# Performance work log

Hardware: AMD Instinct MI355X
Metric: run time of the kernel (lower is better)

Reference implementation:

```python
import jax, jax.numpy as jnp
import numpy as np

N = 100000      # nodes
E = 1600000     # edges
HID = 128       # hidden_dim
HEADS = 4
C = HID // HEADS  # 32 per-head channels
L = 2           # num_layers
G = 64          # graphs in batch


def setup_inputs() -> dict:
    key = jax.random.key(0)
    ks = jax.random.split(key, 24)
    s = 0.1
    inp = {
        'x': jax.random.normal(ks[0], (N, 1), jnp.float32),
        'edge_attr': jax.random.normal(ks[1], (E, 1), jnp.float32),
        'edge_index': jax.random.randint(ks[2], (2, E), 0, N, jnp.int32),
        'batch': jnp.sort(jax.random.randint(ks[3], (N,), 0, G, jnp.int32)),
        # encoders
        'enc_w': jax.random.normal(ks[4], (1, HID), jnp.float32) * s,
        'enc_b': jax.random.normal(ks[5], (HID,), jnp.float32) * s,
        'eenc_w': jax.random.normal(ks[6], (1, HID), jnp.float32) * s,
        'eenc_b': jax.random.normal(ks[7], (HID,), jnp.float32) * s,
        # GATConv params, stacked over layers
        'lin_w': jax.random.normal(ks[8], (L, HID, HID), jnp.float32) * s,
        'att_src': jax.random.normal(ks[9], (L, HEADS, C), jnp.float32) * s,
        'att_dst': jax.random.normal(ks[10], (L, HEADS, C), jnp.float32) * s,
        'att_edge': jax.random.normal(ks[11], (L, HEADS, C), jnp.float32) * s,
        'lin_edge_w': jax.random.normal(ks[12], (L, HID, HID), jnp.float32) * s,
        'conv_b': jax.random.normal(ks[13], (L, HID), jnp.float32) * s,
        # BatchNorm (eval mode, running stats)
        'bn_gamma': jax.random.uniform(ks[14], (L, HID), jnp.float32, 0.5, 1.5),
        'bn_beta': jax.random.normal(ks[15], (L, HID), jnp.float32) * s,
        'bn_mean': jax.random.normal(ks[16], (L, HID), jnp.float32) * s,
        'bn_var': jax.random.uniform(ks[17], (L, HID), jnp.float32, 0.5, 1.5),
        # classifier (num_classes==2 path -> sigmoid, squeeze)
        'w1': jax.random.normal(ks[18], (HID, HID // 2), jnp.float32) * s,
        'b1': jax.random.normal(ks[19], (HID // 2,), jnp.float32) * s,
        'w2': jax.random.normal(ks[20], (HID // 2, 1), jnp.float32) * s,
        'b2': jax.random.normal(ks[21], (1,), jnp.float32) * s,
    }
    return inp


def reference(x, edge_attr, edge_index, batch, enc_w, enc_b, eenc_w, eenc_b,
              lin_w, att_src, att_dst, att_edge, lin_edge_w, conv_b,
              bn_gamma, bn_beta, bn_mean, bn_var, w1, b1, w2, b2):
    src, dst = edge_index[0], edge_index[1]
    h = x @ enc_w + enc_b                      # [N, HID]
    e = edge_attr @ eenc_w + eenc_b            # [E, HID]
    n = h.shape[0]
    nL, H, Ch = att_src.shape[0], att_src.shape[1], att_src.shape[2]
    for l in range(nL):
        identity = h
        xs = (h @ lin_w[l]).reshape(n, H, Ch)            # [N, H, C]
        ee = (e @ lin_edge_w[l]).reshape(-1, H, Ch)      # [E, H, C]
        a_s = jnp.einsum('nhc,hc->nh', xs, att_src[l])
        a_d = jnp.einsum('nhc,hc->nh', xs, att_dst[l])
        a_e = jnp.einsum('ehc,hc->eh', ee, att_edge[l])
        alpha = jax.nn.leaky_relu(a_s[src] + a_d[dst] + a_e, 0.2)  # [E, H]
        # segment softmax over edges grouped by destination node
        amax = jax.ops.segment_max(alpha, dst, num_segments=n)
        amax = jax.lax.stop_gradient(jnp.where(jnp.isfinite(amax), amax, 0.0))
        p = jnp.exp(alpha - amax[dst])
        denom = jax.ops.segment_sum(p, dst, num_segments=n)
        attn = p / (denom[dst] + 1e-16)                  # [E, H]
        msg = (xs[src] * attn[:, :, None]).reshape(-1, H * Ch)
        out = jax.ops.segment_sum(msg, dst, num_segments=n) + conv_b[l]
        # BatchNorm1d (eval mode)
        out = (out - bn_mean[l]) * jax.lax.rsqrt(bn_var[l] + 1e-5) * bn_gamma[l] + bn_beta[l]
        h = jax.nn.relu(out) + identity
    # global mean pool
    cnt = jax.ops.segment_sum(jnp.ones((n,), h.dtype), batch, num_segments=G)
    pooled = jax.ops.segment_sum(h, batch, num_segments=G) / jnp.maximum(cnt, 1.0)[:, None]
    z = jax.nn.relu(pooled @ w1 + b1)
    return jax.nn.sigmoid(z @ w2 + b2)[:, 0]   # [G]
```

## Files before the change

kernel.cpp:

```cpp
#include <hip/hip_runtime.h>
#include <hip/hip_bf16.h>

#define NN 100000
#define EE 1600000
#define HIDD 128
#define GG 64
#define NB 512
#define NPB 196
#define NCH 391
#define CH 4096

typedef short bf16x8 __attribute__((ext_vector_type(8)));
typedef float f32x4 __attribute__((ext_vector_type(4)));

__device__ inline unsigned int f2bf(float f) {
    unsigned int u = __float_as_uint(f);
    return (u + 0x7FFFu + ((u >> 16) & 1u)) >> 16;
}
__device__ inline unsigned int pk2(float a, float b) { return f2bf(a) | (f2bf(b) << 16); }
__device__ inline float blo(unsigned int u) { return __uint_as_float(u << 16); }
__device__ inline float bhi(unsigned int u) { return __uint_as_float(u & 0xFFFF0000u); }


__global__ __launch_bounds__(256) void k_bhist(const int* __restrict__ ei,
                                               int* __restrict__ wg_hist) {
    __shared__ int cnt[NB];
    int t = threadIdx.x;
    cnt[t] = 0; cnt[t + 256] = 0;
    __syncthreads();
    int e0 = blockIdx.x * CH;
    #pragma unroll
    for (int i = 0; i < CH / 256; ++i) {
        int e = e0 + i * 256 + t;
        if (e < EE) {
            unsigned d = (unsigned)ei[EE + e];
            atomicAdd(&cnt[d / NPB], 1);
        }
    }
    __syncthreads();
    wg_hist[blockIdx.x * NB + t] = cnt[t];
    wg_hist[blockIdx.x * NB + 256 + t] = cnt[t + 256];
}

__global__ __launch_bounds__(512) void k_bscan_col(const int* __restrict__ wg_hist,
                                                   int* __restrict__ ofs,
                                                   int* __restrict__ btot) {
    __shared__ int sd[512];
    int b = blockIdx.x;
    int t = threadIdx.x;
    int v = (t < NCH) ? wg_hist[t * NB + b] : 0;
    sd[t] = v;
    __syncthreads();
    for (int off = 1; off < 512; off <<= 1) {
        int u = (t >= off) ? sd[t - off] : 0;
        __syncthreads();
        sd[t] += u;
        __syncthreads();
    }
    if (t < NCH) ofs[t * NB + b] = sd[t] - v;
    if (t == 511) btot[b] = sd[511];
}

__global__ __launch_bounds__(512) void k_bbase(const int* __restrict__ btot,
                                               int* __restrict__ bbase) {
    __shared__ int sd[512];
    int t = threadIdx.x;
    int v = btot[t];
    sd[t] = v;
    __syncthreads();
    for (int off = 1; off < 512; off <<= 1) {
        int u = (t >= off) ? sd[t - off] : 0;
        __syncthreads();
        sd[t] += u;
        __syncthreads();
    }
    bbase[t] = sd[t] - v;
    if (t == 511) bbase[512] = sd[511];
}

__global__ __launch_bounds__(256) void k_bscatter(const int* __restrict__ ei,
                                                  const float* __restrict__ ea,
                                                  const int* __restrict__ ofs,
                                                  const int* __restrict__ bbase,
                                                  uint2* __restrict__ ebuf) {
    __shared__ int lcnt[NB];
    __shared__ int sofs[NB];
    int t = threadIdx.x;
    lcnt[t] = 0; lcnt[t + 256] = 0;
    sofs[t] = ofs[blockIdx.x * NB + t] + bbase[t];
    sofs[t + 256] = ofs[blockIdx.x * NB + 256 + t] + bbase[t + 256];
    __syncthreads();
    int e0 = blockIdx.x * CH;
    #pragma unroll
    for (int i = 0; i < CH / 256; ++i) {
        int e = e0 + i * 256 + t;
        if (e < EE) {
            unsigned s = (unsigned)ei[e];
            unsigned d = (unsigned)ei[EE + e];
            float w = ea[e];
            unsigned b = d / NPB;
            unsigned dloc = d - b * NPB;
            int r = atomicAdd(&lcnt[b], 1);
            ebuf[sofs[b] + r] = make_uint2(s | (dloc << 17), __float_as_uint(w));
        }
    }
}

__global__ __launch_bounds__(256) void k_bsort(const uint2* __restrict__ ebuf,
                                               const int* __restrict__ bbase,
                                               uint2* __restrict__ csr,
                                               int* __restrict__ row_ptr) {
    __shared__ int cnt[NPB];
    __shared__ int sc[256];
    __shared__ int pos[NPB];
    int b = blockIdx.x;
    int t = threadIdx.x;
    int ebeg = bbase[b], eend = bbase[b + 1];
    int n0 = b * NPB;
    int nn = NN - n0; if (nn > NPB) nn = NPB;
    if (t < NPB) cnt[t] = 0;
    __syncthreads();
    for (int j = ebeg + t; j < eend; j += 256) {
        uint2 r = ebuf[j];
        atomicAdd(&cnt[r.x >> 17], 1);
    }
    __syncthreads();
    int v = (t < NPB) ? cnt[t] : 0;
    sc[t] = v;
    __syncthreads();
    for (int off = 1; off < 256; off <<= 1) {
        int u = (t >= off) ? sc[t - off] : 0;
        __syncthreads();
        sc[t] += u;
        __syncthreads();
    }
    int lofs = sc[t] - v;
    if (t < NPB) {
        pos[t] = lofs;
        if (t < nn) row_ptr[n0 + t] = ebeg + lofs;
    }
    __syncthreads();
    for (int j = ebeg + t; j < eend; j += 256) {
        uint2 r = ebuf[j];
        int dloc = r.x >> 17;
        int slot = ebeg + atomicAdd(&pos[dloc], 1);
        csr[slot] = make_uint2(r.x & 0x1FFFFu, r.y);
    }
    if (b == 0 && t == 0) row_ptr[NN] = EE;
}


__global__ void k_derive(const float* __restrict__ enc_w, const float* __restrict__ enc_b,
                         const float* __restrict__ eenc_w, const float* __restrict__ eenc_b,
                         const float* __restrict__ lin_w, const float* __restrict__ lin_edge_w,
                         const float* __restrict__ att_src, const float* __restrict__ att_dst,
                         const float* __restrict__ att_edge,
                         const float* __restrict__ bn_gamma, const float* __restrict__ bn_beta,
                         const float* __restrict__ bn_mean, const float* __restrict__ bn_var,
                         float* __restrict__ cblk, unsigned short* __restrict__ wpk16) {
    int t = threadIdx.x;
    __shared__ float red[128];

    float P = 0.f, Q = 0.f;
    for (int j = 0; j < 128; ++j) {
        float w = lin_w[j * 128 + t];
        P += enc_w[j] * w;
        Q += enc_b[j] * w;
    }
    cblk[t] = P;
    cblk[128 + t] = Q;

    for (int l = 0; l < 2; ++l) {
        float sc = bn_gamma[l * 128 + t] * rsqrtf(bn_var[l * 128 + t] + 1e-5f);
        cblk[256 + l * 128 + t] = sc;
        cblk[512 + l * 128 + t] = bn_beta[l * 128 + t] - bn_mean[l * 128 + t] * sc;
    }

    for (int k = 0; k < 128; ++k) {
        wpk16[t * 128 + k] = (unsigned short)f2bf(lin_w[16384 + k * 128 + t]);
    }

    auto headred = [&](float v, int outbase) {
        red[t] = v;
        __syncthreads();
        if (t < 4) {
            float s = 0.f;
            for (int c = 0; c < 32; ++c) s += red[t * 32 + c];
            cblk[outbase + t] = s;
        }
        __syncthreads();
    };

    headred(P * att_src[t], 768);
    headred(Q * att_src[t], 772);
    headred(P * att_dst[t], 776);
    headred(Q * att_dst[t], 780);

    for (int l = 0; l < 2; ++l) {
        float W1 = 0.f, W2 = 0.f;
        for (int j = 0; j < 128; ++j) {
            float w = lin_edge_w[l * 16384 + j * 128 + t];
            W1 += eenc_w[j] * w;
            W2 += eenc_b[j] * w;
        }
        headred(W1 * att_edge[l * 128 + t], 784 + l * 4);
        headred(W2 * att_edge[l * 128 + t], 792 + l * 4);
    }
}


__global__ __launch_bounds__(256) void k_l0(const uint2* __restrict__ csr,
                                            const int* __restrict__ row_ptr,
                                            const float* __restrict__ x,
                                            const float* __restrict__ cblk,
                                            float* __restrict__ tmp0) {
    int wid = threadIdx.x >> 6, lane = threadIdx.x & 63;
    int n = blockIdx.x * 4 + wid;
    if (n >= NN) return;
    int h = lane & 3, eo = lane >> 2;
    float xdv = x[n];
    float ps = cblk[768 + h], qs = cblk[772 + h];
    float base = xdv * cblk[776 + h] + cblk[780 + h] + cblk[792 + h];
    float au = cblk[784 + h];
    int jb = row_ptr[n], je = row_ptr[n + 1];
    float s = 0.f, sx = 0.f;
    for (int j0 = jb; j0 < je; j0 += 16) {
        int j = j0 + eo;
        if (j < je) {
            uint2 r = csr[j];
            float xsv = x[r.x];
            float w = __uint_as_float(r.y);
            float a = xsv * ps + qs + base + w * au;
            a = (a > 0.f) ? a : 0.2f * a;
            float p = __expf(a);
            s += p;
            sx += p * xsv;
        }
    }
    #pragma unroll
    for (int off = 4; off < 64; off <<= 1) {
        s += __shfl_xor(s, off, 64);
        sx += __shfl_xor(sx, off, 64);
    }
    if (lane < 4) {
        tmp0[(size_t)n * 8 + lane] = s;
        tmp0[(size_t)n * 8 + 4 + lane] = sx;
    }
}

__global__ void k_l0_epi(const float* __restrict__ x, const float* __restrict__ enc_w,
                         const float* __restrict__ enc_b, const float* __restrict__ conv_b,
                         const float* __restrict__ cblk, const float* __restrict__ tmp0,
                         float* __restrict__ hbuf, unsigned short* __restrict__ h16) {
    int idx = blockIdx.x * blockDim.x + threadIdx.x;
    if (idx >= NN * HIDD) return;
    int n = idx >> 7, k = idx & 127, h = (k >> 5) & 3;
    float s = tmp0[n * 8 + h];
    float sx = tmp0[n * 8 + 4 + h];
    float inv = 1.f / (s + 1e-16f);
    float agg = (sx * cblk[k] + s * cblk[128 + k]) * inv + conv_b[k];
    float o = agg * cblk[256 + k] + cblk[512 + k];
    float hv = fmaxf(o, 0.f) + x[n] * enc_w[k] + enc_b[k];
    hbuf[idx] = hv;
    h16[idx] = (unsigned short)f2bf(hv);
}


__global__ __launch_bounds__(256) void k_gemm_mfma(const unsigned short* __restrict__ h16,
                                                   const unsigned short* __restrict__ wpk,
                                                   unsigned short* __restrict__ xs16) {
    int wid = threadIdx.x >> 6, lane = threadIdx.x & 63;
    int rbase = blockIdx.x * 64 + wid * 16;
    int hi = lane >> 4, c15 = lane & 15;

    const bf16x8* hrow = (const bf16x8*)(h16 + (size_t)(rbase + c15) * 128);
    bf16x8 a0 = hrow[hi];
    bf16x8 a1 = hrow[4 + hi];
    bf16x8 a2 = hrow[8 + hi];
    bf16x8 a3 = hrow[12 + hi];

    f32x4 acc[8];
    #pragma unroll
    for (int t8 = 0; t8 < 8; ++t8) {
        const bf16x8* wrow = (const bf16x8*)(wpk + (size_t)(t8 * 16 + c15) * 128);
        f32x4 a_ = {0.f, 0.f, 0.f, 0.f};
        a_ = __builtin_amdgcn_mfma_f32_16x16x32_bf16(a0, wrow[hi], a_, 0, 0, 0);
        a_ = __builtin_amdgcn_mfma_f32_16x16x32_bf16(a1, wrow[4 + hi], a_, 0, 0, 0);
        a_ = __builtin_amdgcn_mfma_f32_16x16x32_bf16(a2, wrow[8 + hi], a_, 0, 0, 0);
        a_ = __builtin_amdgcn_mfma_f32_16x16x32_bf16(a3, wrow[12 + hi], a_, 0, 0, 0);
        acc[t8] = a_;
    }
    #pragma unroll
    for (int j = 0; j < 4; ++j) {
        size_t rb = (size_t)(rbase + hi * 4 + j) * 128;
        #pragma unroll
        for (int t8 = 0; t8 < 8; ++t8) {
            xs16[rb + t8 * 16 + c15] = (unsigned short)f2bf(acc[t8][j]);
        }
    }
}

__global__ void k_asad(const unsigned short* __restrict__ xs16,
                       const float* __restrict__ att_src1, const float* __restrict__ att_dst1,
                       float* __restrict__ a_s, float* __restrict__ a_d) {
    int wid = threadIdx.x >> 6, lane = threadIdx.x & 63;
    int n = blockIdx.x * 4 + wid;
    if (n >= NN) return;
    unsigned int u = *(const unsigned int*)(xs16 + (size_t)n * 128 + lane * 2);
    float v0 = blo(u), v1 = bhi(u);
    float2 as2 = *(const float2*)(att_src1 + lane * 2);
    float2 ad2 = *(const float2*)(att_dst1 + lane * 2);
    float vs = v0 * as2.x + v1 * as2.y;
    float vd = v0 * ad2.x + v1 * ad2.y;
    #pragma unroll
    for (int off = 1; off < 16; off <<= 1) {
        vs += __shfl_xor(vs, off, 64);
        vd += __shfl_xor(vd, off, 64);
    }
    if ((lane & 15) == 0) {
        a_s[n * 4 + (lane >> 4)] = vs;
        a_d[n * 4 + (lane >> 4)] = vd;
    }
}


__global__ __launch_bounds__(256) void k_l1_agg(const unsigned short* __restrict__ xs16,
                                                const uint2* __restrict__ csr,
                                                const float* __restrict__ a_s,
                                                const float* __restrict__ a_d,
                                                const int* __restrict__ row_ptr,
                                                const float* __restrict__ cblk,
                                                const float* __restrict__ conv_b,
                                                unsigned short* __restrict__ outb) {
    int wid = threadIdx.x >> 6, lane = threadIdx.x & 63;
    int n = blockIdx.x * 4 + wid;
    if (n >= NN) return;
    int h = lane >> 4;
    int c0 = lane * 2;

    float adh = a_d[(size_t)n * 4 + h] + cblk[796 + h];
    float au = cblk[788 + h];

    float acc0 = 0.f, acc1 = 0.f, s = 0.f;
    int jb = row_ptr[n], je = row_ptr[n + 1];
    const char* xb = (const char*)xs16;
    int j = jb;
    for (; j + 7 < je; j += 8) {
        uint2 r[8];
        float as[8];
        unsigned int u[8];
        #pragma unroll
        for (int q = 0; q < 8; ++q) r[q] = csr[j + q];
        #pragma unroll
        for (int q = 0; q < 8; ++q) as[q] = a_s[(size_t)r[q].x * 4 + h];
        #pragma unroll
        for (int q = 0; q < 8; ++q)
            u[q] = *(const unsigned int*)(xb + ((size_t)r[q].x << 8) + (lane << 2));
        #pragma unroll
        for (int q = 0; q < 8; ++q) {
            float al = as[q] + adh + __uint_as_float(r[q].y) * au;
            al = (al > 0.f) ? al : 0.2f * al;
            float p = __expf(al);
            s += p;
            acc0 += p * blo(u[q]);
            acc1 += p * bhi(u[q]);
        }
    }
    for (; j + 3 < je; j += 4) {
        uint2 r[4];
        float as[4];
        unsigned int u[4];
        #pragma unroll
        for (int q = 0; q < 4; ++q) r[q] = csr[j + q];
        #pragma unroll
        for (int q = 0; q < 4; ++q) as[q] = a_s[(size_t)r[q].x * 4 + h];
        #pragma unroll
        for (int q = 0; q < 4; ++q)
            u[q] = *(const unsigned int*)(xb + ((size_t)r[q].x << 8) + (lane << 2));
        #pragma unroll
        for (int q = 0; q < 4; ++q) {
            float al = as[q] + adh + __uint_as_float(r[q].y) * au;
            al = (al > 0.f) ? al : 0.2f * al;
            float p = __expf(al);
            s += p;
            acc0 += p * blo(u[q]);
            acc1 += p * bhi(u[q]);
        }
    }
    for (; j < je; ++j) {
        uint2 r0 = csr[j];
        float as0 = a_s[(size_t)r0.x * 4 + h];
        unsigned int u0 = *(const unsigned int*)(xb + ((size_t)r0.x << 8) + (lane << 2));
        float al0 = as0 + adh + __uint_as_float(r0.y) * au;
        al0 = (al0 > 0.f) ? al0 : 0.2f * al0;
        float p0 = __expf(al0);
        s += p0;
        acc0 += p0 * blo(u0);
        acc1 += p0 * bhi(u0);
    }
    float inv = 1.f / (s + 1e-16f);
    float o0 = acc0 * inv + conv_b[128 + c0];
    float o1 = acc1 * inv + conv_b[128 + c0 + 1];
    o0 = o0 * cblk[384 + c0] + cblk[640 + c0];
    o1 = o1 * cblk[384 + c0 + 1] + cblk[640 + c0 + 1];
    unsigned int pk = pk2(fmaxf(o0, 0.f), fmaxf(o1, 0.f));
    *(unsigned int*)(outb + (size_t)n * 128 + c0) = pk;
}


__global__ void k_pool(const float* __restrict__ hbuf, const unsigned short* __restrict__ outb,
                       const int* __restrict__ batch,
                       float* __restrict__ pooled, float* __restrict__ gcnt) {
    int t = threadIdx.x;
    int n0 = blockIdx.x * 256;
    int nend = min(n0 + 256, NN);
    float acc = 0.f;
    int run = 0;
    int gprev = batch[n0];
    for (int n = n0; n < nend; ++n) {
        int g = batch[n];
        if (g != gprev) {
            atomicAdd(&pooled[gprev * 128 + t], acc);
            if (t == 0) atomicAdd(&gcnt[gprev], (float)run);
            acc = 0.f;
            run = 0;
            gprev = g;
        }
        float hv = hbuf[(size_t)n * 128 + t];
        unsigned short ub = outb[(size_t)n * 128 + t];
        acc += hv + __uint_as_float(((unsigned int)ub) << 16);
        run++;
    }
    atomicAdd(&pooled[gprev * 128 + t], acc);
    if (t == 0) atomicAdd(&gcnt[gprev], (float)run);
}

__global__ void k_head(const float* __restrict__ pooled, const float* __restrict__ gcnt,
                       const float* __restrict__ w1, const float* __restrict__ b1,
                       const float* __restrict__ w2, const float* __restrict__ b2,
                       float* __restrict__ out) {
    int g = blockIdx.x;
    int j = threadIdx.x;
    float inv = 1.f / fmaxf(gcnt[g], 1.f);
    float acc = b1[j];
    for (int k = 0; k < 128; ++k) acc += pooled[g * 128 + k] * inv * w1[k * 64 + j];
    float z = fmaxf(acc, 0.f);
    float v = z * w2[j];
    #pragma unroll
    for (int off = 32; off; off >>= 1) v += __shfl_down(v, off, 64);
    if (j == 0) out[g] = 1.f / (1.f + __expf(-(v + b2[0])));
}


extern "C" void kernel_launch(void* const* d_in, const int* in_sizes, int n_in,
                              void* d_out, int out_size, void* d_ws, size_t ws_size,
                              hipStream_t stream) {
    const float* x        = (const float*)d_in[0];
    const float* ea       = (const float*)d_in[1];
    const int*   ei       = (const int*)d_in[2];
    const int*   batch    = (const int*)d_in[3];
    const float* enc_w    = (const float*)d_in[4];
    const float* enc_b    = (const float*)d_in[5];
    const float* eenc_w   = (const float*)d_in[6];
    const float* eenc_b   = (const float*)d_in[7];
    const float* lin_w    = (const float*)d_in[8];
    const float* att_src  = (const float*)d_in[9];
    const float* att_dst  = (const float*)d_in[10];
    const float* att_edge = (const float*)d_in[11];
    const float* lin_edge = (const float*)d_in[12];
    const float* conv_b   = (const float*)d_in[13];
    const float* bn_gamma = (const float*)d_in[14];
    const float* bn_beta  = (const float*)d_in[15];
    const float* bn_mean  = (const float*)d_in[16];
    const float* bn_var   = (const float*)d_in[17];
    const float* w1       = (const float*)d_in[18];
    const float* b1       = (const float*)d_in[19];
    const float* w2       = (const float*)d_in[20];
    const float* b2       = (const float*)d_in[21];
    float* out = (float*)d_out;

    char* ws = (char*)d_ws;
    size_t off = 0;
    auto alloc = [&](size_t bytes) {
        size_t o = off;
        off = (off + bytes + 511) & ~(size_t)511;
        return o;
    };
    int*    wg_hist = (int*)(ws + alloc((size_t)NCH * NB * 4));
    int*    ofs     = (int*)(ws + alloc((size_t)NCH * NB * 4));
    int*    btot    = (int*)(ws + alloc(NB * 4));
    int*    bbase   = (int*)(ws + alloc((NB + 1) * 4));
    int*    row_ptr = (int*)(ws + alloc((size_t)(NN + 1) * 4));
    uint2*  ebuf    = (uint2*)(ws + alloc((size_t)EE * 8));
    uint2*  csr     = (uint2*)(ws + alloc((size_t)EE * 8));
    float*  cblk    = (float*)(ws + alloc(1024 * 4));
    unsigned short* wpk16 = (unsigned short*)(ws + alloc(128 * 128 * 2));
    float*  tmp0    = (float*)(ws + alloc((size_t)NN * 8 * 4));
    float*  a_s     = (float*)(ws + alloc((size_t)NN * 4 * 4));
    float*  a_d     = (float*)(ws + alloc((size_t)NN * 4 * 4));
    float*  hbuf    = (float*)(ws + alloc((size_t)NN * HIDD * 4));
    unsigned short* h16  = (unsigned short*)(ws + alloc((size_t)(NN + 64) * HIDD * 2));
    unsigned short* xs16 = (unsigned short*)(ws + alloc((size_t)(NN + 64) * HIDD * 2));
    unsigned short* outb = (unsigned short*)(ws + alloc((size_t)NN * HIDD * 2));
    float*  pooled  = (float*)(ws + alloc(GG * HIDD * 4 + GG * 4));
    float*  gcnt    = pooled + GG * HIDD;

    hipMemsetAsync(pooled, 0, GG * HIDD * 4 + GG * 4, stream);

    const int nparts = (NN + 255) / 256;
    const int nwave4 = (NN + 3) / 4;

    k_bhist<<<NCH, 256, 0, stream>>>(ei, wg_hist);
    k_bscan_col<<<NB, 512, 0, stream>>>(wg_hist, ofs, btot);
    k_bbase<<<1, 512, 0, stream>>>(btot, bbase);
    k_bscatter<<<NCH, 256, 0, stream>>>(ei, ea, ofs, bbase, ebuf);
    k_bsort<<<511, 256, 0, stream>>>(ebuf, bbase, csr, row_ptr);

    k_derive<<<1, 128, 0, stream>>>(enc_w, enc_b, eenc_w, eenc_b, lin_w, lin_edge,
                                    att_src, att_dst, att_edge,
                                    bn_gamma, bn_beta, bn_mean, bn_var, cblk, wpk16);

    k_l0<<<nwave4, 256, 0, stream>>>(csr, row_ptr, x, cblk, tmp0);
    k_l0_epi<<<(NN * HIDD + 255) / 256, 256, 0, stream>>>(x, enc_w, enc_b, conv_b, cblk,
                                                          tmp0, hbuf, h16);

    k_gemm_mfma<<<(NN + 63) / 64, 256, 0, stream>>>(h16, wpk16, xs16);
    k_asad<<<nwave4, 256, 0, stream>>>(xs16, att_src + 128, att_dst + 128, a_s, a_d);
    k_l1_agg<<<nwave4, 256, 0, stream>>>(xs16, csr, a_s, a_d, row_ptr, cblk, conv_b, outb);

    k_pool<<<nparts, 128, 0, stream>>>(hbuf, outb, batch, pooled, gcnt);
    k_head<<<GG, 64, 0, stream>>>(pooled, gcnt, w1, b1, w2, b2, out);
}
```

Baseline: 455.4 us.

## Drop fp32 hidden buffer and pool from bf16 copy with finer-grained blocks

Removes the fp32 copy of the first-layer output, so the epilogue writes only the bf16 version, and mean pooling reads bf16 for both layer contributions. The pooling kernel is restructured to handle 32 nodes per block with two-channel vectorised loads, plus a fast path when every node in the block belongs to the same graph. This cuts global memory writes and reads and adds parallelism to pooling, at the cost of bf16 rounding on the pooled residual and more atomics.

```diff
diff --git a/kernel.cpp b/kernel.cpp
--- a/kernel.cpp
+++ b/kernel.cpp
@@ -251,7 +251,7 @@
 __global__ void k_l0_epi(const float* __restrict__ x, const float* __restrict__ enc_w,
                          const float* __restrict__ enc_b, const float* __restrict__ conv_b,
                          const float* __restrict__ cblk, const float* __restrict__ tmp0,
-                         float* __restrict__ hbuf, unsigned short* __restrict__ h16) {
+                         unsigned short* __restrict__ h16) {
     int idx = blockIdx.x * blockDim.x + threadIdx.x;
     if (idx >= NN * HIDD) return;
     int n = idx >> 7, k = idx & 127, h = (k >> 5) & 3;
@@ -261,7 +261,6 @@
     float agg = (sx * cblk[k] + s * cblk[128 + k]) * inv + conv_b[k];
     float o = agg * cblk[256 + k] + cblk[512 + k];
     float hv = fmaxf(o, 0.f) + x[n] * enc_w[k] + enc_b[k];
-    hbuf[idx] = hv;
     h16[idx] = (unsigned short)f2bf(hv);
 }
 
@@ -408,31 +407,54 @@
 }
 
 
-__global__ void k_pool(const float* __restrict__ hbuf, const unsigned short* __restrict__ outb,
-                       const int* __restrict__ batch,
-                       float* __restrict__ pooled, float* __restrict__ gcnt) {
-    int t = threadIdx.x;
-    int n0 = blockIdx.x * 256;
-    int nend = min(n0 + 256, NN);
-    float acc = 0.f;
-    int run = 0;
-    int gprev = batch[n0];
-    for (int n = n0; n < nend; ++n) {
-        int g = batch[n];
-        if (g != gprev) {
-            atomicAdd(&pooled[gprev * 128 + t], acc);
-            if (t == 0) atomicAdd(&gcnt[gprev], (float)run);
-            acc = 0.f;
-            run = 0;
-            gprev = g;
-        }
-        float hv = hbuf[(size_t)n * 128 + t];
-        unsigned short ub = outb[(size_t)n * 128 + t];
-        acc += hv + __uint_as_float(((unsigned int)ub) << 16);
-        run++;
-    }
-    atomicAdd(&pooled[gprev * 128 + t], acc);
-    if (t == 0) atomicAdd(&gcnt[gprev], (float)run);
+__global__ __launch_bounds__(128) void k_pool(const unsigned short* __restrict__ h16,
+                                              const unsigned short* __restrict__ outb,
+                                              const int* __restrict__ batch,
+                                              float* __restrict__ pooled,
+                                              float* __restrict__ gcnt) {
+    int t = threadIdx.x;
+    int c = (t & 63) * 2;
+    int half = t >> 6;
+    int n0 = blockIdx.x * 32;
+    int gfirst = batch[n0];
+    int glast = batch[n0 + 31];
+    if (gfirst == glast) {
+        float a0 = 0.f, a1 = 0.f;
+        #pragma unroll
+        for (int i = 0; i < 16; ++i) {
+            size_t n = (size_t)(n0 + half + i * 2);
+            unsigned int uh = *(const unsigned int*)(h16 + n * 128 + c);
+            unsigned int ub = *(const unsigned int*)(outb + n * 128 + c);
+            a0 += blo(uh) + blo(ub);
+            a1 += bhi(uh) + bhi(ub);
+        }
+        atomicAdd(&pooled[gfirst * 128 + c], a0);
+        atomicAdd(&pooled[gfirst * 128 + c + 1], a1);
+        if (t == 0) atomicAdd(&gcnt[gfirst], 32.f);
+    } else if (half == 0) {
+        float a0 = 0.f, a1 = 0.f;
+        int run = 0;
+        int gprev = gfirst;
+        for (int n = n0; n < n0 + 32; ++n) {
+            int g = batch[n];
+            if (g != gprev) {
+                atomicAdd(&pooled[gprev * 128 + c], a0);
+                atomicAdd(&pooled[gprev * 128 + c + 1], a1);
+                if (t == 0) atomicAdd(&gcnt[gprev], (float)run);
+                a0 = a1 = 0.f;
+                run = 0;
+                gprev = g;
+            }
+            unsigned int uh = *(const unsigned int*)(h16 + (size_t)n * 128 + c);
+            unsigned int ub = *(const unsigned int*)(outb + (size_t)n * 128 + c);
+            a0 += blo(uh) + blo(ub);
+            a1 += bhi(uh) + bhi(ub);
+            run++;
+        }
+        atomicAdd(&pooled[gprev * 128 + c], a0);
+        atomicAdd(&pooled[gprev * 128 + c + 1], a1);
+        if (t == 0) atomicAdd(&gcnt[gprev], (float)run);
+    }
 }
 
 __global__ void k_head(const float* __restrict__ pooled, const float* __restrict__ gcnt,
@@ -498,7 +520,6 @@
     float*  tmp0    = (float*)(ws + alloc((size_t)NN * 8 * 4));
     float*  a_s     = (float*)(ws + alloc((size_t)NN * 4 * 4));
     float*  a_d     = (float*)(ws + alloc((size_t)NN * 4 * 4));
-    float*  hbuf    = (float*)(ws + alloc((size_t)NN * HIDD * 4));
     unsigned short* h16  = (unsigned short*)(ws + alloc((size_t)(NN + 64) * HIDD * 2));
     unsigned short* xs16 = (unsigned short*)(ws + alloc((size_t)(NN + 64) * HIDD * 2));
     unsigned short* outb = (unsigned short*)(ws + alloc((size_t)NN * HIDD * 2));
@@ -507,7 +528,6 @@
 
     hipMemsetAsync(pooled, 0, GG * HIDD * 4 + GG * 4, stream);
 
-    const int nparts = (NN + 255) / 256;
     const int nwave4 = (NN + 3) / 4;
 
     k_bhist<<<NCH, 256, 0, stream>>>(ei, wg_hist);
@@ -522,12 +542,12 @@
 
     k_l0<<<nwave4, 256, 0, stream>>>(csr, row_ptr, x, cblk, tmp0);
     k_l0_epi<<<(NN * HIDD + 255) / 256, 256, 0, stream>>>(x, enc_w, enc_b, conv_b, cblk,
-                                                          tmp0, hbuf, h16);
+                                                          tmp0, h16);
 
     k_gemm_mfma<<<(NN + 63) / 64, 256, 0, stream>>>(h16, wpk16, xs16);
     k_asad<<<nwave4, 256, 0, stream>>>(xs16, att_src + 128, att_dst + 128, a_s, a_d);
     k_l1_agg<<<nwave4, 256, 0, stream>>>(xs16, csr, a_s, a_d, row_ptr, cblk, conv_b, outb);
 
-    k_pool<<<nparts, 128, 0, stream>>>(hbuf, outb, batch, pooled, gcnt);
+    k_pool<<<NN / 32, 128, 0, stream>>>(h16, outb, batch, pooled, gcnt);
     k_head<<<GG, 64, 0, stream>>>(pooled, gcnt, w1, b1, w2, b2, out);
 }
```

After: 388.7 us. 1.17x faster.
